# Kernel optimization log

Measured on AMD Instinct MI355X. Metric: run time of the kernel, lower is better.

## Reference

```python
import jax, jax.numpy as jnp
import numpy as np

IN_DIM = 256
OUT_DIM = 64   # per-head dim
NUM_HEADS = 8
B = 8
N = 1024


def setup_inputs() -> dict:
    key = jax.random.key(0)
    k_adj, k_h, kq, kk, kv, kbq, kbk, kbv = jax.random.split(key, 8)
    adj_matrix = jax.random.randint(k_adj, (N, N), 0, 2, dtype=jnp.int32)
    h = jax.random.normal(k_h, (B, N, IN_DIM), dtype=jnp.float32)
    s = 1.0 / np.sqrt(IN_DIM)
    Wq = jax.random.normal(kq, (IN_DIM, OUT_DIM * NUM_HEADS), dtype=jnp.float32) * s
    Wk = jax.random.normal(kk, (IN_DIM, OUT_DIM * NUM_HEADS), dtype=jnp.float32) * s
    Wv = jax.random.normal(kv, (IN_DIM, OUT_DIM * NUM_HEADS), dtype=jnp.float32) * s
    bq = jax.random.normal(kbq, (OUT_DIM * NUM_HEADS,), dtype=jnp.float32) * 0.01
    bk = jax.random.normal(kbk, (OUT_DIM * NUM_HEADS,), dtype=jnp.float32) * 0.01
    bv = jax.random.normal(kbv, (OUT_DIM * NUM_HEADS,), dtype=jnp.float32) * 0.01
    return {"adj_matrix": adj_matrix, "h": h, "Wq": Wq, "bq": bq,
            "Wk": Wk, "bk": bk, "Wv": Wv, "bv": bv}


def reference(adj_matrix, h, Wq, bq, Wk, bk, Wv, bv):
    B_, N_, _ = h.shape
    H, D = NUM_HEADS, OUT_DIM
    Qh = (h @ Wq + bq).reshape(B_, N_, H, D)
    Kh = (h @ Wk + bk).reshape(B_, N_, H, D)
    Vh = (h @ Wv + bv).reshape(B_, N_, H, D)
    scores = jnp.einsum('bnhd,bmhd->bhnm', Qh, Kh) / jnp.sqrt(jnp.float32(D))
    # adjacency mask broadcast over batch and heads (neigh_attention=True)
    scores = jnp.where(adj_matrix[None, None, :, :] == 0, -jnp.inf, scores)
    attn = jax.nn.softmax(scores, axis=-1)
    out = jnp.einsum('bhnm,bmhd->bnhd', attn, Vh)
    return out.reshape(B_, N_, H * D)
```

## Files before the change

kernel.cpp:

```cpp
#include <hip/hip_runtime.h>
#include <hip/hip_bf16.h>
#include <math.h>

#define IN_DIM 256
#define HD     512
#define NHEADS 8
#define DH     64
#define NSEQ   1024
#define BATCH  8

#define QSCALE  0.18033688011112042f
#define MASKVAL -3.0e38f

typedef unsigned short u16;
typedef unsigned int   u32;
typedef short bf16x8 __attribute__((ext_vector_type(8)));
typedef float f32x4  __attribute__((ext_vector_type(4)));

#if __has_builtin(__builtin_amdgcn_exp2f)
#define EXP2(x) __builtin_amdgcn_exp2f(x)
#else
#define EXP2(x) __expf(0.69314718056f * (x))
#endif

static __device__ __forceinline__ u16 f2bf(float x) {
    u32 u = __builtin_bit_cast(u32, x);
    u += 0x7FFFu + ((u >> 16) & 1u);
    return (u16)(u >> 16);
}
static __device__ __forceinline__ u32 pk(u16 a, u16 b) {
    return (u32)a | ((u32)b << 16);
}
static __device__ __forceinline__ u32 cvtpk(float a, float b) {
    __hip_bfloat162 t = __float22bfloat162_rn(make_float2(a, b));
    u32 r; __builtin_memcpy(&r, &t, 4);
    return r;
}

__global__ __launch_bounds__(256)
void prep_kernel(const float* __restrict__ Wq, const float* __restrict__ Wk,
                 const float* __restrict__ Wv, const int* __restrict__ adj,
                 u16* __restrict__ Wt, float* __restrict__ MaddF)
{
    __shared__ u32 shpool[64 * 65];
    const int bid = blockIdx.x, tid = threadIdx.x;

    if (bid < 96) {
        float* tile = (float*)shpool;
        const int wk = bid;
        const int k0 = (wk & 3) * 64, n0 = ((wk >> 2) & 7) * 64, wsel = wk >> 5;
        const float* W = (wsel == 0) ? Wq : (wsel == 1) ? Wk : Wv;
        u16* Out = Wt + (size_t)wsel * HD * IN_DIM;

        const int r = tid >> 2, c0 = (tid & 3) * 16;
#pragma unroll
        for (int j = 0; j < 16; j += 4) {
            float4 v = *(const float4*)(W + (size_t)(k0 + r) * HD + n0 + c0 + j);
            tile[r * 65 + c0 + j + 0] = v.x; tile[r * 65 + c0 + j + 1] = v.y;
            tile[r * 65 + c0 + j + 2] = v.z; tile[r * 65 + c0 + j + 3] = v.w;
        }
        __syncthreads();
        const int n = tid >> 2, ks = (tid & 3) * 16;
        u16 o[16];
#pragma unroll
        for (int j = 0; j < 16; ++j) o[j] = f2bf(tile[(ks + j) * 65 + n]);
        uint4 u0, u1;
        u0.x = pk(o[0], o[1]);   u0.y = pk(o[2], o[3]);
        u0.z = pk(o[4], o[5]);   u0.w = pk(o[6], o[7]);
        u1.x = pk(o[8], o[9]);   u1.y = pk(o[10], o[11]);
        u1.z = pk(o[12], o[13]); u1.w = pk(o[14], o[15]);
        u16* dst = Out + (size_t)(n0 + n) * IN_DIM + k0 + ks;
        *(uint4*)(dst) = u0;
        *(uint4*)(dst + 8) = u1;
    } else {
        int* tile = (int*)shpool;
        const int abid = bid - 96;
        const int tR = abid >> 4, tC = abid & 15;
        const int r = tid >> 2, cg = (tid & 3) * 16;
        const int* src = adj + (size_t)(tR * 64 + r) * NSEQ + tC * 64 + cg;
#pragma unroll
        for (int j = 0; j < 16; j += 4) {
            int4 a = *(const int4*)(src + j);
            tile[r * 65 + cg + j + 0] = a.x; tile[r * 65 + cg + j + 1] = a.y;
            tile[r * 65 + cg + j + 2] = a.z; tile[r * 65 + cg + j + 3] = a.w;
        }
        __syncthreads();
        const int kk = tid >> 2, qg = (tid & 3) * 16;
        float* dst = MaddF + (size_t)(tC * 64 + kk) * NSEQ + tR * 64 + qg;
#pragma unroll
        for (int j = 0; j < 16; j += 4) {
            float4 o;
            o.x = (tile[(qg + j + 0) * 65 + kk] == 0) ? MASKVAL : 0.f;
            o.y = (tile[(qg + j + 1) * 65 + kk] == 0) ? MASKVAL : 0.f;
            o.z = (tile[(qg + j + 2) * 65 + kk] == 0) ? MASKVAL : 0.f;
            o.w = (tile[(qg + j + 3) * 65 + kk] == 0) ? MASKVAL : 0.f;
            *(float4*)(dst + j) = o;
        }
    }
}

__global__ __launch_bounds__(256, 4)
void qkv_gemm_kernel(const float* __restrict__ h, const u16* __restrict__ Wt,
                     const float* __restrict__ bq, const float* __restrict__ bk,
                     const float* __restrict__ bv,
                     u16* __restrict__ Qg, u16* __restrict__ Kg,
                     u16* __restrict__ Vtg)
{
    __shared__ u16 pool[64 * 64 + 3 * 64 * 64];
    u16* As = pool;
    u16* Bs = pool + 64 * 64;

    const int m0 = blockIdx.x * 64;
    const int hh = blockIdx.y;
    const int n0 = hh * 64;

    const int tid = threadIdx.x;
    const int w = tid >> 6, lane = tid & 63, l15 = lane & 15, quad = lane >> 4;
    const int sw = l15 & 7;

    f32x4 acc[3][4];
#pragma unroll
    for (int wh = 0; wh < 3; ++wh)
#pragma unroll
        for (int t = 0; t < 4; ++t) acc[wh][t] = (f32x4){0.f, 0.f, 0.f, 0.f};

    const int arow = tid >> 2, acg = (tid & 3) * 2;
    const int brow = tid & 63, bgrp = tid >> 6;
    const float* srcA = h + (size_t)(m0 + arow) * IN_DIM;

    for (int kk = 0; kk < IN_DIM; kk += 64) {
        __syncthreads();
#pragma unroll
        for (int g = 0; g < 2; ++g) {
            const float* p = srcA + kk + (acg + g) * 8;
            float4 v0 = *(const float4*)(p);
            float4 v1 = *(const float4*)(p + 4);
            uint4 u;
            u.x = cvtpk(v0.x, v0.y); u.y = cvtpk(v0.z, v0.w);
            u.z = cvtpk(v1.x, v1.y); u.w = cvtpk(v1.z, v1.w);
            *(uint4*)&As[arow * 64 + (((acg + g) ^ (arow & 7)) * 8)] = u;
        }
#pragma unroll
        for (int i = 0; i < 6; ++i) {
            const int gc = bgrp * 6 + i;
            const int wh = gc >> 3, c8 = gc & 7;
            *(uint4*)&Bs[wh * 4096 + brow * 64 + ((c8 ^ (brow & 7)) * 8)] =
                *(const uint4*)(Wt + (size_t)wh * HD * IN_DIM +
                                (size_t)(n0 + brow) * IN_DIM + kk + c8 * 8);
        }
        __syncthreads();
        const int ra = (w * 16 + l15) * 64;
        bf16x8 a0 = *(const bf16x8*)&As[ra + ((quad ^ sw) * 8)];
        bf16x8 a1 = *(const bf16x8*)&As[ra + (((4 + quad) ^ sw) * 8)];
#pragma unroll
        for (int t = 0; t < 4; ++t) {
            const int rb = (t * 16 + l15) * 64;
#pragma unroll
            for (int wh = 0; wh < 3; ++wh) {
                bf16x8 b0 = *(const bf16x8*)&Bs[wh * 4096 + rb + ((quad ^ sw) * 8)];
                bf16x8 b1 = *(const bf16x8*)&Bs[wh * 4096 + rb + (((4 + quad) ^ sw) * 8)];
                acc[wh][t] = __builtin_amdgcn_mfma_f32_16x16x32_bf16(a0, b0, acc[wh][t], 0, 0, 0);
                acc[wh][t] = __builtin_amdgcn_mfma_f32_16x16x32_bf16(a1, b1, acc[wh][t], 0, 0, 0);
            }
        }
    }

    for (int which = 0; which < 2; ++which) {
        u16* T = pool;
        const float* bias = (which == 0) ? bq : bk;
        u16* Out = (which == 0) ? Qg : Kg;
        const float scale = (which == 0) ? QSCALE : 1.0f;
        __syncthreads();
#pragma unroll
        for (int t = 0; t < 4; ++t) {
            const float bvv = bias[n0 + t * 16 + l15];
            const int rowb = w * 16 + quad * 4;
#pragma unroll
            for (int r = 0; r < 4; ++r)
                T[(rowb + r) * 72 + t * 16 + l15] =
                    f2bf((acc[which][t][r] + bvv) * scale);
        }
        __syncthreads();
        const int row = tid >> 2, qc = (tid & 3) * 16;
        u16* dst = Out + (size_t)(m0 + row) * HD + n0 + qc;
        const u16* srcT = &T[row * 72 + qc];
        *(uint4*)(dst)     = *(const uint4*)(srcT);
        *(uint4*)(dst + 8) = *(const uint4*)(srcT + 8);
    }

    {
        u16* T = pool;
        __syncthreads();
#pragma unroll
        for (int t = 0; t < 4; ++t) {
            const float bvv = bv[n0 + t * 16 + l15];
            const int trow = (t * 16 + l15) * 72;
#pragma unroll
            for (int r = 0; r < 4; ++r)
                T[trow + (quad * 4 + r) * 4 + w] = f2bf(acc[2][t][r] + bvv);
        }
        __syncthreads();
        const int b = m0 >> 10, nloc = m0 & 1023;
        const int d = tid >> 2, c = (tid & 3) * 16;
        u16* dst = Vtg + ((size_t)(b * NHEADS + hh) * DH + d) * NSEQ + nloc + c;
        *(uint4*)(dst)     = *(uint4*)&T[d * 72 + c];
        *(uint4*)(dst + 8) = *(uint4*)&T[d * 72 + c + 8];
    }
}

__global__ __launch_bounds__(512, 4)
void attn_kernel(const float* __restrict__ MaddF, const u16* __restrict__ Qg,
                 const u16* __restrict__ Kg, const u16* __restrict__ Vtg,
                 float* __restrict__ out)
{
    __shared__ u16 Ks[2][64 * 64];
    __shared__ u16 Vs[2][64 * 64];
    __shared__ u16 Ps[128 * 64];

    const int tid = threadIdx.x;
    const int w = tid >> 6, lane = tid & 63, l15 = lane & 15, quad = lane >> 4;
    const int bh = blockIdx.x, qt = blockIdx.y;
    const int b = bh >> 3;
    const int n0 = qt * 128;
    const size_t rowbase = (size_t)b * NSEQ;
    const int colbase = (bh & 7) * DH;
    const int sw = l15 & 7;

    const u16* qrow = Qg + (rowbase + n0 + w * 16 + l15) * HD + colbase;
    const bf16x8 qa0 = *(const bf16x8*)(qrow + quad * 8);
    const bf16x8 qa1 = *(const bf16x8*)(qrow + 32 + quad * 8);

    const int srow = tid >> 3, c8w = tid & 7;
    const int swc = ((c8w ^ (srow & 7)) * 8);
    const u16* kgp = Kg + (rowbase + srow) * HD + colbase + c8w * 8;
    const u16* vgp = Vtg + ((size_t)bh * DH + srow) * NSEQ + c8w * 8;
    const float* mgp = MaddF + (size_t)l15 * NSEQ + n0 + w * 16 + quad * 4;

    uint4 kG = *(const uint4*)kgp;
    uint4 vG = *(const uint4*)vgp;
    float4 mG[4];
#pragma unroll
    for (int t = 0; t < 4; ++t) mG[t] = *(const float4*)(mgp + (size_t)(t * 16) * NSEQ);

    *(uint4*)&Ks[0][srow * 64 + swc] = kG;
    *(uint4*)&Vs[0][srow * 64 + swc] = vG;
    __syncthreads();

    float lrow[4] = {0.f, 0.f, 0.f, 0.f};
    f32x4 O[4];
#pragma unroll
    for (int t = 0; t < 4; ++t) O[t] = (f32x4){0.f, 0.f, 0.f, 0.f};

    const int pwbase = (w * 16 + quad * 4) * 64;
    const int parow  = (w * 16 + l15) * 64;

    for (int ch = 0; ch < 16; ++ch) {
        const int cur = ch & 1;

        f32x4 s4[4];
#pragma unroll
        for (int t = 0; t < 4; ++t)
            s4[t] = (f32x4){mG[t].x, mG[t].y, mG[t].z, mG[t].w};

        if (ch < 15) {
            kG = *(const uint4*)(kgp + (size_t)(ch + 1) * 64 * HD);
            vG = *(const uint4*)(vgp + (ch + 1) * 64);
#pragma unroll
            for (int t = 0; t < 4; ++t)
                mG[t] = *(const float4*)(mgp + ((size_t)(ch + 1) * 64 + t * 16) * NSEQ);
        }

#pragma unroll
        for (int t = 0; t < 4; ++t) {
            const int rb = (t * 16 + l15) * 64;
            bf16x8 kb0 = *(const bf16x8*)&Ks[cur][rb + ((quad ^ sw) * 8)];
            bf16x8 kb1 = *(const bf16x8*)&Ks[cur][rb + (((4 + quad) ^ sw) * 8)];
            s4[t] = __builtin_amdgcn_mfma_f32_16x16x32_bf16(qa0, kb0, s4[t], 0, 0, 0);
            s4[t] = __builtin_amdgcn_mfma_f32_16x16x32_bf16(qa1, kb1, s4[t], 0, 0, 0);
        }

        if (ch < 15) {
            *(uint4*)&Ks[1 - cur][srow * 64 + swc] = kG;
            *(uint4*)&Vs[1 - cur][srow * 64 + swc] = vG;
        }

#pragma unroll
        for (int r = 0; r < 4; ++r) {
            float p0 = EXP2(s4[0][r]);
            float p1 = EXP2(s4[1][r]);
            float p2 = EXP2(s4[2][r]);
            float p3 = EXP2(s4[3][r]);
            lrow[r] += (p0 + p1) + (p2 + p3);
            uint2 pw;
            pw.x = cvtpk(p0, p1);
            pw.y = cvtpk(p2, p3);
            const int q7 = (quad * 4 + r) & 7;
            *(uint2*)&Ps[pwbase + r * 64 + (((l15 >> 1) ^ q7) * 8) + (l15 & 1) * 4] = pw;
        }

        {
            bf16x8 pa0 = *(const bf16x8*)&Ps[parow + ((quad ^ sw) * 8)];
            bf16x8 pa1 = *(const bf16x8*)&Ps[parow + (((4 + quad) ^ sw) * 8)];
#pragma unroll
            for (int t = 0; t < 4; ++t) {
                const int rb = (t * 16 + l15) * 64;
                bf16x8 vb0 = *(const bf16x8*)&Vs[cur][rb + ((quad ^ sw) * 8)];
                bf16x8 vb1 = *(const bf16x8*)&Vs[cur][rb + (((4 + quad) ^ sw) * 8)];
                O[t] = __builtin_amdgcn_mfma_f32_16x16x32_bf16(pa0, vb0, O[t], 0, 0, 0);
                O[t] = __builtin_amdgcn_mfma_f32_16x16x32_bf16(pa1, vb1, O[t], 0, 0, 0);
            }
        }
        __syncthreads();
    }

#pragma unroll
    for (int d = 1; d < 16; d <<= 1)
#pragma unroll
        for (int r = 0; r < 4; ++r)
            lrow[r] += __shfl_xor(lrow[r], d, 64);

    float inv[4];
#pragma unroll
    for (int r = 0; r < 4; ++r) inv[r] = 1.0f / lrow[r];
#pragma unroll
    for (int t = 0; t < 4; ++t)
#pragma unroll
        for (int r = 0; r < 4; ++r)
            out[(rowbase + n0 + w * 16 + quad * 4 + r) * HD + colbase + t * 16 + l15] =
                O[t][r] * inv[r];
}

extern "C" void kernel_launch(void* const* d_in, const int* in_sizes, int n_in,
                              void* d_out, int out_size, void* d_ws, size_t ws_size,
                              hipStream_t stream) {
    const int*   adj = (const int*)d_in[0];
    const float* h   = (const float*)d_in[1];
    const float* Wq  = (const float*)d_in[2];
    const float* bq  = (const float*)d_in[3];
    const float* Wk  = (const float*)d_in[4];
    const float* bk  = (const float*)d_in[5];
    const float* Wv  = (const float*)d_in[6];
    const float* bv  = (const float*)d_in[7];
    float* outp = (float*)d_out;

    u16* Wt     = (u16*)d_ws;
    u16* Qg     = Wt + (size_t)3 * HD * IN_DIM;
    u16* Kg     = Qg + (size_t)BATCH * NSEQ * HD;
    u16* Vtg    = Kg + (size_t)BATCH * NSEQ * HD;
    float* MaddF = (float*)(Vtg + (size_t)BATCH * NSEQ * HD);

    prep_kernel<<<352, 256, 0, stream>>>(Wq, Wk, Wv, adj, Wt, MaddF);
    qkv_gemm_kernel<<<dim3(BATCH * NSEQ / 64, NHEADS), 256, 0, stream>>>(
        h, Wt, bq, bk, bv, Qg, Kg, Vtg);
    attn_kernel<<<dim3(BATCH * NHEADS, NSEQ / 128), 512, 0, stream>>>(
        MaddF, Qg, Kg, Vtg, outp);
}
```

Before: 140.9 us.

## Store mask as bf16, fold mask prep into GEMM grid, halve attention tile

The adjacency mask is now stored as a transposed bf16 additive bias (0xFF7F, about -3.39e38) instead of fp32, which halves the mask traffic read by every attention block. The mask transpose now runs in two extra grid rows of the QKV GEMM launch, so it overlaps with the GEMM instead of running in its own prep kernel with the weight transpose. The attention kernel drops to 64 query rows per block with 256 threads, doubling the block count, while each thread loads two 16-byte K/V chunks. In exchange, every block rereads K/V per query tile, so global K/V traffic doubles.

```diff
diff --git a/kernel.cpp b/kernel.cpp
--- a/kernel.cpp
+++ b/kernel.cpp
@@ -9,8 +9,7 @@
 #define NSEQ   1024
 #define BATCH  8
 
-#define QSCALE  0.18033688011112042f
-#define MASKVAL -3.0e38f
+#define QSCALE 0.18033688011112042f
 
 typedef unsigned short u16;
 typedef unsigned int   u32;
@@ -28,6 +27,9 @@
     u += 0x7FFFu + ((u >> 16) & 1u);
     return (u16)(u >> 16);
 }
+static __device__ __forceinline__ float bf2f(u16 x) {
+    return __builtin_bit_cast(float, ((u32)x) << 16);
+}
 static __device__ __forceinline__ u32 pk(u16 a, u16 b) {
     return (u32)a | ((u32)b << 16);
 }
@@ -38,75 +40,77 @@
 }
 
 __global__ __launch_bounds__(256)
-void prep_kernel(const float* __restrict__ Wq, const float* __restrict__ Wk,
-                 const float* __restrict__ Wv, const int* __restrict__ adj,
-                 u16* __restrict__ Wt, float* __restrict__ MaddF)
+void wtrans_kernel(const float* __restrict__ Wq, const float* __restrict__ Wk,
+                   const float* __restrict__ Wv, u16* __restrict__ Wt)
 {
-    __shared__ u32 shpool[64 * 65];
+    __shared__ float tile[64 * 65];
     const int bid = blockIdx.x, tid = threadIdx.x;
-
-    if (bid < 96) {
-        float* tile = (float*)shpool;
-        const int wk = bid;
-        const int k0 = (wk & 3) * 64, n0 = ((wk >> 2) & 7) * 64, wsel = wk >> 5;
-        const float* W = (wsel == 0) ? Wq : (wsel == 1) ? Wk : Wv;
-        u16* Out = Wt + (size_t)wsel * HD * IN_DIM;
-
-        const int r = tid >> 2, c0 = (tid & 3) * 16;
+    const int k0 = (bid & 3) * 64, n0 = ((bid >> 2) & 7) * 64, wsel = bid >> 5;
+    const float* W = (wsel == 0) ? Wq : (wsel == 1) ? Wk : Wv;
+    u16* Out = Wt + (size_t)wsel * HD * IN_DIM;
+
+    const int r = tid >> 2, c0 = (tid & 3) * 16;
+#pragma unroll
+    for (int j = 0; j < 16; j += 4) {
+        float4 v = *(const float4*)(W + (size_t)(k0 + r) * HD + n0 + c0 + j);
+        tile[r * 65 + c0 + j + 0] = v.x; tile[r * 65 + c0 + j + 1] = v.y;
+        tile[r * 65 + c0 + j + 2] = v.z; tile[r * 65 + c0 + j + 3] = v.w;
+    }
+    __syncthreads();
+    const int n = tid >> 2, ks = (tid & 3) * 16;
+    u16 o[16];
+#pragma unroll
+    for (int j = 0; j < 16; ++j) o[j] = f2bf(tile[(ks + j) * 65 + n]);
+    uint4 u0, u1;
+    u0.x = pk(o[0], o[1]);   u0.y = pk(o[2], o[3]);
+    u0.z = pk(o[4], o[5]);   u0.w = pk(o[6], o[7]);
+    u1.x = pk(o[8], o[9]);   u1.y = pk(o[10], o[11]);
+    u1.z = pk(o[12], o[13]); u1.w = pk(o[14], o[15]);
+    u16* dst = Out + (size_t)(n0 + n) * IN_DIM + k0 + ks;
+    *(uint4*)(dst) = u0;
+    *(uint4*)(dst + 8) = u1;
+}
+
+__global__ __launch_bounds__(256, 4)
+void gemm_mask_kernel(const float* __restrict__ h, const u16* __restrict__ Wt,
+                      const int* __restrict__ adj,
+                      const float* __restrict__ bq, const float* __restrict__ bk,
+                      const float* __restrict__ bv,
+                      u16* __restrict__ Qg, u16* __restrict__ Kg,
+                      u16* __restrict__ Vtg, u16* __restrict__ MaddT)
+{
+    __shared__ u16 pool[64 * 64 + 3 * 64 * 64];
+    const int tid = threadIdx.x;
+
+    if (blockIdx.y >= 8) {
+        int* tile = (int*)pool;
+        const int abid = (blockIdx.y - 8) * 128 + blockIdx.x;
+        const int tR = abid >> 4, tC = abid & 15;
+        const int r = tid >> 2, cg = (tid & 3) * 16;
+        const int* src = adj + (size_t)(tR * 64 + r) * NSEQ + tC * 64 + cg;
 #pragma unroll
         for (int j = 0; j < 16; j += 4) {
-            float4 v = *(const float4*)(W + (size_t)(k0 + r) * HD + n0 + c0 + j);
-            tile[r * 65 + c0 + j + 0] = v.x; tile[r * 65 + c0 + j + 1] = v.y;
-            tile[r * 65 + c0 + j + 2] = v.z; tile[r * 65 + c0 + j + 3] = v.w;
-        }
-        __syncthreads();
-        const int n = tid >> 2, ks = (tid & 3) * 16;
+            int4 a = *(const int4*)(src + j);
+            tile[r * 65 + cg + j + 0] = a.x; tile[r * 65 + cg + j + 1] = a.y;
+            tile[r * 65 + cg + j + 2] = a.z; tile[r * 65 + cg + j + 3] = a.w;
+        }
+        __syncthreads();
+        const int kk = tid >> 2, qg = (tid & 3) * 16;
         u16 o[16];
 #pragma unroll
-        for (int j = 0; j < 16; ++j) o[j] = f2bf(tile[(ks + j) * 65 + n]);
+        for (int j = 0; j < 16; ++j)
+            o[j] = (tile[(qg + j) * 65 + kk] == 0) ? (u16)0xFF7F : (u16)0;
         uint4 u0, u1;
         u0.x = pk(o[0], o[1]);   u0.y = pk(o[2], o[3]);
         u0.z = pk(o[4], o[5]);   u0.w = pk(o[6], o[7]);
         u1.x = pk(o[8], o[9]);   u1.y = pk(o[10], o[11]);
         u1.z = pk(o[12], o[13]); u1.w = pk(o[14], o[15]);
-        u16* dst = Out + (size_t)(n0 + n) * IN_DIM + k0 + ks;
+        u16* dst = MaddT + (size_t)(tC * 64 + kk) * NSEQ + tR * 64 + qg;
         *(uint4*)(dst) = u0;
         *(uint4*)(dst + 8) = u1;
-    } else {
-        int* tile = (int*)shpool;
-        const int abid = bid - 96;
-        const int tR = abid >> 4, tC = abid & 15;
-        const int r = tid >> 2, cg = (tid & 3) * 16;
-        const int* src = adj + (size_t)(tR * 64 + r) * NSEQ + tC * 64 + cg;
-#pragma unroll
-        for (int j = 0; j < 16; j += 4) {
-            int4 a = *(const int4*)(src + j);
-            tile[r * 65 + cg + j + 0] = a.x; tile[r * 65 + cg + j + 1] = a.y;
-            tile[r * 65 + cg + j + 2] = a.z; tile[r * 65 + cg + j + 3] = a.w;
-        }
-        __syncthreads();
-        const int kk = tid >> 2, qg = (tid & 3) * 16;
-        float* dst = MaddF + (size_t)(tC * 64 + kk) * NSEQ + tR * 64 + qg;
-#pragma unroll
-        for (int j = 0; j < 16; j += 4) {
-            float4 o;
-            o.x = (tile[(qg + j + 0) * 65 + kk] == 0) ? MASKVAL : 0.f;
-            o.y = (tile[(qg + j + 1) * 65 + kk] == 0) ? MASKVAL : 0.f;
-            o.z = (tile[(qg + j + 2) * 65 + kk] == 0) ? MASKVAL : 0.f;
-            o.w = (tile[(qg + j + 3) * 65 + kk] == 0) ? MASKVAL : 0.f;
-            *(float4*)(dst + j) = o;
-        }
-    }
-}
-
-__global__ __launch_bounds__(256, 4)
-void qkv_gemm_kernel(const float* __restrict__ h, const u16* __restrict__ Wt,
-                     const float* __restrict__ bq, const float* __restrict__ bk,
-                     const float* __restrict__ bv,
-                     u16* __restrict__ Qg, u16* __restrict__ Kg,
-                     u16* __restrict__ Vtg)
-{
-    __shared__ u16 pool[64 * 64 + 3 * 64 * 64];
+        return;
+    }
+
     u16* As = pool;
     u16* Bs = pool + 64 * 64;
 
@@ -114,7 +118,6 @@
     const int hh = blockIdx.y;
     const int n0 = hh * 64;
 
-    const int tid = threadIdx.x;
     const int w = tid >> 6, lane = tid & 63, l15 = lane & 15, quad = lane >> 4;
     const int sw = l15 & 7;
 
@@ -208,20 +211,20 @@
     }
 }
 
-__global__ __launch_bounds__(512, 4)
-void attn_kernel(const float* __restrict__ MaddF, const u16* __restrict__ Qg,
+__global__ __launch_bounds__(256, 4)
+void attn_kernel(const u16* __restrict__ MaddT, const u16* __restrict__ Qg,
                  const u16* __restrict__ Kg, const u16* __restrict__ Vtg,
                  float* __restrict__ out)
 {
     __shared__ u16 Ks[2][64 * 64];
     __shared__ u16 Vs[2][64 * 64];
-    __shared__ u16 Ps[128 * 64];
+    __shared__ u16 Ps[64 * 64];
 
     const int tid = threadIdx.x;
     const int w = tid >> 6, lane = tid & 63, l15 = lane & 15, quad = lane >> 4;
     const int bh = blockIdx.x, qt = blockIdx.y;
     const int b = bh >> 3;
-    const int n0 = qt * 128;
+    const int n0 = qt * 64;
     const size_t rowbase = (size_t)b * NSEQ;
     const int colbase = (bh & 7) * DH;
     const int sw = l15 & 7;
@@ -230,20 +233,22 @@
     const bf16x8 qa0 = *(const bf16x8*)(qrow + quad * 8);
     const bf16x8 qa1 = *(const bf16x8*)(qrow + 32 + quad * 8);
 
-    const int srow = tid >> 3, c8w = tid & 7;
-    const int swc = ((c8w ^ (srow & 7)) * 8);
-    const u16* kgp = Kg + (rowbase + srow) * HD + colbase + c8w * 8;
-    const u16* vgp = Vtg + ((size_t)bh * DH + srow) * NSEQ + c8w * 8;
-    const float* mgp = MaddF + (size_t)l15 * NSEQ + n0 + w * 16 + quad * 4;
-
-    uint4 kG = *(const uint4*)kgp;
-    uint4 vG = *(const uint4*)vgp;
-    float4 mG[4];
-#pragma unroll
-    for (int t = 0; t < 4; ++t) mG[t] = *(const float4*)(mgp + (size_t)(t * 16) * NSEQ);
-
-    *(uint4*)&Ks[0][srow * 64 + swc] = kG;
-    *(uint4*)&Vs[0][srow * 64 + swc] = vG;
+    const int srow = tid >> 2, cp = (tid & 3) * 2;
+    const int swc0 = ((cp ^ (srow & 7)) * 8), swc1 = (((cp + 1) ^ (srow & 7)) * 8);
+    const u16* kgp = Kg + (rowbase + srow) * HD + colbase + cp * 8;
+    const u16* vgp = Vtg + ((size_t)bh * DH + srow) * NSEQ + cp * 8;
+    const u16* mgp = MaddT + (size_t)l15 * NSEQ + n0 + w * 16 + quad * 4;
+
+    uint4 kG0 = *(const uint4*)kgp, kG1 = *(const uint4*)(kgp + 8);
+    uint4 vG0 = *(const uint4*)vgp, vG1 = *(const uint4*)(vgp + 8);
+    ushort4 mG[4];
+#pragma unroll
+    for (int t = 0; t < 4; ++t) mG[t] = *(const ushort4*)(mgp + (size_t)(t * 16) * NSEQ);
+
+    *(uint4*)&Ks[0][srow * 64 + swc0] = kG0;
+    *(uint4*)&Ks[0][srow * 64 + swc1] = kG1;
+    *(uint4*)&Vs[0][srow * 64 + swc0] = vG0;
+    *(uint4*)&Vs[0][srow * 64 + swc1] = vG1;
     __syncthreads();
 
     float lrow[4] = {0.f, 0.f, 0.f, 0.f};
@@ -260,14 +265,17 @@
         f32x4 s4[4];
 #pragma unroll
         for (int t = 0; t < 4; ++t)
-            s4[t] = (f32x4){mG[t].x, mG[t].y, mG[t].z, mG[t].w};
+            s4[t] = (f32x4){bf2f(mG[t].x), bf2f(mG[t].y),
+                            bf2f(mG[t].z), bf2f(mG[t].w)};
 
         if (ch < 15) {
-            kG = *(const uint4*)(kgp + (size_t)(ch + 1) * 64 * HD);
-            vG = *(const uint4*)(vgp + (ch + 1) * 64);
+            kG0 = *(const uint4*)(kgp + (size_t)(ch + 1) * 64 * HD);
+            kG1 = *(const uint4*)(kgp + (size_t)(ch + 1) * 64 * HD + 8);
+            vG0 = *(const uint4*)(vgp + (ch + 1) * 64);
+            vG1 = *(const uint4*)(vgp + (ch + 1) * 64 + 8);
 #pragma unroll
             for (int t = 0; t < 4; ++t)
-                mG[t] = *(const float4*)(mgp + ((size_t)(ch + 1) * 64 + t * 16) * NSEQ);
+                mG[t] = *(const ushort4*)(mgp + ((size_t)(ch + 1) * 64 + t * 16) * NSEQ);
         }
 
 #pragma unroll
@@ -280,8 +288,10 @@
         }
 
         if (ch < 15) {
-            *(uint4*)&Ks[1 - cur][srow * 64 + swc] = kG;
-            *(uint4*)&Vs[1 - cur][srow * 64 + swc] = vG;
+            *(uint4*)&Ks[1 - cur][srow * 64 + swc0] = kG0;
+            *(uint4*)&Ks[1 - cur][srow * 64 + swc1] = kG1;
+            *(uint4*)&Vs[1 - cur][srow * 64 + swc0] = vG0;
+            *(uint4*)&Vs[1 - cur][srow * 64 + swc1] = vG1;
         }
 
 #pragma unroll
@@ -343,15 +353,15 @@
     const float* bv  = (const float*)d_in[7];
     float* outp = (float*)d_out;
 
-    u16* Wt     = (u16*)d_ws;
-    u16* Qg     = Wt + (size_t)3 * HD * IN_DIM;
-    u16* Kg     = Qg + (size_t)BATCH * NSEQ * HD;
-    u16* Vtg    = Kg + (size_t)BATCH * NSEQ * HD;
-    float* MaddF = (float*)(Vtg + (size_t)BATCH * NSEQ * HD);
-
-    prep_kernel<<<352, 256, 0, stream>>>(Wq, Wk, Wv, adj, Wt, MaddF);
-    qkv_gemm_kernel<<<dim3(BATCH * NSEQ / 64, NHEADS), 256, 0, stream>>>(
-        h, Wt, bq, bk, bv, Qg, Kg, Vtg);
-    attn_kernel<<<dim3(BATCH * NHEADS, NSEQ / 128), 512, 0, stream>>>(
-        MaddF, Qg, Kg, Vtg, outp);
-}
+    u16* Wt    = (u16*)d_ws;
+    u16* Qg    = Wt + (size_t)3 * HD * IN_DIM;
+    u16* Kg    = Qg + (size_t)BATCH * NSEQ * HD;
+    u16* Vtg   = Kg + (size_t)BATCH * NSEQ * HD;
+    u16* MaddT = Vtg + (size_t)BATCH * NSEQ * HD;
+
+    wtrans_kernel<<<96, 256, 0, stream>>>(Wq, Wk, Wv, Wt);
+    gemm_mask_kernel<<<dim3(BATCH * NSEQ / 64, 10), 256, 0, stream>>>(
+        h, Wt, adj, bq, bk, bv, Qg, Kg, Vtg, MaddT);
+    attn_kernel<<<dim3(BATCH * NHEADS, NSEQ / 64), 256, 0, stream>>>(
+        MaddT, Qg, Kg, Vtg, outp);
+}
```

Result: no change. 143.4 us (+1.8%).
